# Kernel tuning notes

Hardware: AMD Instinct MI355X
Metric: run time of the kernel (lower is better)

Reference implementation:

```python
import jax, jax.numpy as jnp
import numpy as np

N_NODES = 100000
N_EDGES = 1600000
IN_FEATS = 256
HEADS = 4
OUT_FEATS = 32
NEG_SLOPE = 0.2


def setup_inputs() -> dict:
    key = jax.random.key(0)
    k = jax.random.split(key, 7)
    feat = jax.random.normal(k[0], (N_NODES, IN_FEATS), dtype=jnp.float32)
    src = jax.random.randint(k[1], (N_EDGES,), 0, N_NODES)
    dst = jax.random.randint(k[2], (N_EDGES,), 0, N_NODES)
    W = jax.random.normal(k[3], (HEADS * OUT_FEATS, IN_FEATS), dtype=jnp.float32) * 0.05
    attn_l = jax.random.normal(k[4], (1, HEADS, OUT_FEATS), dtype=jnp.float32) * 0.1
    attn_r = jax.random.normal(k[5], (1, HEADS, OUT_FEATS), dtype=jnp.float32) * 0.1
    bias = jnp.zeros((HEADS * OUT_FEATS,), dtype=jnp.float32)
    return {"feat": feat, "src": src, "dst": dst, "W": W,
            "attn_l": attn_l, "attn_r": attn_r, "bias": bias}


def reference(feat, src, dst, W, attn_l, attn_r, bias):
    N = feat.shape[0]
    H, F = attn_l.shape[1], attn_l.shape[2]
    # linear projection: [N, H*F] -> [N, H, F]
    ft = (feat @ W.T).reshape(N, H, F)
    # per-node attention scores [N, H]
    el = jnp.sum(ft * attn_l, axis=-1)
    er = jnp.sum(ft * attn_r, axis=-1)
    # edge scores: u_add_v + LeakyReLU, [E, H]
    e = el[src] + er[dst]
    e = jnp.where(e >= 0, e, NEG_SLOPE * e)
    # edge softmax segmented by destination node
    emax = jax.ops.segment_max(e, dst, num_segments=N)  # [N, H]
    emax = jnp.where(jnp.isfinite(emax), emax, 0.0)
    ex = jnp.exp(e - emax[dst])  # [E, H]
    esum = jax.ops.segment_sum(ex, dst, num_segments=N)  # [N, H]
    a = ex / jnp.maximum(esum[dst], 1e-16)  # [E, H]
    # weighted scatter-sum aggregation: u_mul_e + sum
    msg = ft[src] * a[:, :, None]  # [E, H, F]
    rst = jax.ops.segment_sum(msg, dst, num_segments=N)  # [N, H, F]
    rst = rst + bias.reshape(1, H, F)
    return rst


if __name__ == "__main__":
    out = reference(**setup_inputs())
    print(out.shape, out.dtype)
```

## Files before the change

### kernel.cpp

```cpp
#include <hip/hip_runtime.h>

#define NEG_SLOPE 0.2f
#define G_SHIFT 8
#define G_SIZE  256
#define NB1     256

typedef __attribute__((ext_vector_type(8))) short short8;
typedef __attribute__((ext_vector_type(4))) float floatx4;

__device__ inline unsigned short f32_to_bf16(float f) {
    union { float f; unsigned int u; } c; c.f = f;
    unsigned int u = c.u;
    u += 0x7FFFu + ((u >> 16) & 1u);
    return (unsigned short)(u >> 16);
}
__device__ inline float bf16_lo(unsigned int u) {
    union { unsigned int u; float f; } c; c.u = u << 16; return c.f;
}
__device__ inline float bf16_hi(unsigned int u) {
    union { unsigned int u; float f; } c; c.u = u & 0xFFFF0000u; return c.f;
}

__global__ __launch_bounds__(256) void k_wconv(const float* __restrict__ W,
                                               unsigned short* __restrict__ Wb,
                                               int n) {
    int i = blockIdx.x * 256 + threadIdx.x;
    if (i < n) Wb[i] = f32_to_bf16(W[i]);
}

__global__ __launch_bounds__(256) void k_gemm_mfma(const float* __restrict__ feat,
                                                   const unsigned short* __restrict__ Wb,
                                                   unsigned short* __restrict__ ftb,
                                                   int M) {
    const int tid  = threadIdx.x;
    const int wave = tid >> 6;
    const int lane = tid & 63;
    const int l16  = lane & 15;
    const int quad = lane >> 4;
    const int mw   = blockIdx.x * 64 + wave * 16;

    int arow = mw + l16;
    if (arow >= M) arow = M - 1;
    const float* aptr = feat + (size_t)arow * 256 + quad * 8;

    floatx4 acc[8];
#pragma unroll
    for (int t = 0; t < 8; ++t) acc[t] = (floatx4){0.f, 0.f, 0.f, 0.f};

#pragma unroll
    for (int k0 = 0; k0 < 256; k0 += 32) {
        float4 a0 = *(const float4*)(aptr + k0);
        float4 a1 = *(const float4*)(aptr + k0 + 4);
        short8 af;
        af[0] = (short)f32_to_bf16(a0.x);
        af[1] = (short)f32_to_bf16(a0.y);
        af[2] = (short)f32_to_bf16(a0.z);
        af[3] = (short)f32_to_bf16(a0.w);
        af[4] = (short)f32_to_bf16(a1.x);
        af[5] = (short)f32_to_bf16(a1.y);
        af[6] = (short)f32_to_bf16(a1.z);
        af[7] = (short)f32_to_bf16(a1.w);
#pragma unroll
        for (int t = 0; t < 8; ++t) {
            short8 bf = *(const short8*)(Wb + (size_t)(t * 16 + l16) * 256 + k0 + quad * 8);
            acc[t] = __builtin_amdgcn_mfma_f32_16x16x32_bf16(af, bf, acc[t], 0, 0, 0);
        }
    }

#pragma unroll
    for (int t = 0; t < 8; ++t) {
#pragma unroll
        for (int r = 0; r < 4; ++r) {
            int row = mw + quad * 4 + r;
            if (row < M)
                ftb[(size_t)row * 128 + t * 16 + l16] = f32_to_bf16(acc[t][r]);
        }
    }
}

__global__ __launch_bounds__(256) void k_elr(const unsigned short* __restrict__ ftb,
                                             const float* __restrict__ al,
                                             const float* __restrict__ ar,
                                             float* __restrict__ el,
                                             float* __restrict__ er,
                                             int NH) {
    int i = blockIdx.x * 256 + threadIdx.x;
    if (i >= NH) return;
    int h = i & 3;
    const unsigned int* f = (const unsigned int*)ftb + (size_t)i * 16;
    const float* lp = al + h * 32;
    const float* rp = ar + h * 32;
    float sl = 0.f, sr = 0.f;
#pragma unroll
    for (int j = 0; j < 16; ++j) {
        unsigned int u = f[j];
        float f0 = bf16_lo(u), f1 = bf16_hi(u);
        sl += f0 * lp[2 * j] + f1 * lp[2 * j + 1];
        sr += f0 * rp[2 * j] + f1 * rp[2 * j + 1];
    }
    el[i] = sl;
    er[i] = sr;
}

__global__ __launch_bounds__(256) void k_count(const int* __restrict__ dst,
                                               int* __restrict__ counts,
                                               int E, int CH, int B) {
    __shared__ int hist[512];
    int j = blockIdx.x, t = threadIdx.x;
    for (int bk = t; bk < B; bk += 256) hist[bk] = 0;
    __syncthreads();
    int lo = j * CH, hi = min(E, lo + CH);
    for (int i = lo + t; i < hi; i += 256)
        atomicAdd(&hist[dst[i] >> G_SHIFT], 1);
    __syncthreads();
    for (int bk = t; bk < B; bk += 256) counts[bk * NB1 + j] = hist[bk];
}

__global__ __launch_bounds__(256) void k_scan1(const int* __restrict__ deg,
                                               int* __restrict__ offs,
                                               int* __restrict__ bsum, int n) {
    __shared__ int ls[256];
    int b = blockIdx.x, t = threadIdx.x;
    int base = b * 1024 + t * 4;
    int d0 = (base + 0 < n) ? deg[base + 0] : 0;
    int d1 = (base + 1 < n) ? deg[base + 1] : 0;
    int d2 = (base + 2 < n) ? deg[base + 2] : 0;
    int d3 = (base + 3 < n) ? deg[base + 3] : 0;
    int s = d0 + d1 + d2 + d3;
    ls[t] = s;
    __syncthreads();
    for (int o = 1; o < 256; o <<= 1) {
        int v = (t >= o) ? ls[t - o] : 0;
        __syncthreads();
        ls[t] += v;
        __syncthreads();
    }
    int excl = ls[t] - s;
    if (base + 0 < n) offs[base + 0] = excl;
    if (base + 1 < n) offs[base + 1] = excl + d0;
    if (base + 2 < n) offs[base + 2] = excl + d0 + d1;
    if (base + 3 < n) offs[base + 3] = excl + d0 + d1 + d2;
    if (t == 255) bsum[b] = ls[255];
}

__global__ __launch_bounds__(256) void k_scan2(int* __restrict__ bsum, int NB) {
    __shared__ int ls[256];
    int t = threadIdx.x;
    int v = (t < NB) ? bsum[t] : 0;
    ls[t] = v;
    __syncthreads();
    for (int o = 1; o < 256; o <<= 1) {
        int u = (t >= o) ? ls[t - o] : 0;
        __syncthreads();
        ls[t] += u;
        __syncthreads();
    }
    if (t < NB) bsum[t] = ls[t] - v;
}

__global__ __launch_bounds__(256) void k_partition(const int* __restrict__ src,
                                                   const int* __restrict__ dst,
                                                   const int* __restrict__ scanned,
                                                   const int* __restrict__ bsum,
                                                   int* __restrict__ part,
                                                   int E, int CH, int B) {
    __shared__ int curs[512];
    int j = blockIdx.x, t = threadIdx.x;
    for (int bk = t; bk < B; bk += 256) {
        int idx = bk * NB1 + j;
        curs[bk] = scanned[idx] + bsum[idx >> 10];
    }
    __syncthreads();
    int lo = j * CH, hi = min(E, lo + CH);
    for (int i = lo + t; i < hi; i += 256) {
        int d = dst[i];
        int bk = d >> G_SHIFT;
        int pos = atomicAdd(&curs[bk], 1);
        if (pos >= 0 && pos < E)
            part[pos] = ((d & (G_SIZE - 1)) << 17) | src[i];
    }
}

__global__ __launch_bounds__(256) void k_bucket(const int* __restrict__ scanned,
                                                const int* __restrict__ bsum,
                                                const int* __restrict__ part,
                                                int* __restrict__ offs,
                                                int* __restrict__ esrc,
                                                int E, int B, int N) {
    __shared__ int hist[256], ls[256], curs[256];
    int b = blockIdx.x, t = threadIdx.x;
    int i0 = b * NB1;
    int start = scanned[i0] + bsum[i0 >> 10];
    int end = E;
    if (b < B - 1) {
        int i1 = (b + 1) * NB1;
        end = scanned[i1] + bsum[i1 >> 10];
    }

    hist[t] = 0;
    __syncthreads();
    for (int i = start + t; i < end; i += 256)
        atomicAdd(&hist[(part[i] >> 17) & 255], 1);
    __syncthreads();

    int h = hist[t];
    ls[t] = h;
    __syncthreads();
    for (int o = 1; o < 256; o <<= 1) {
        int v = (t >= o) ? ls[t - o] : 0;
        __syncthreads();
        ls[t] += v;
        __syncthreads();
    }
    int excl = ls[t] - h;
    curs[t] = excl;
    int node = b * G_SIZE + t;
    if (node < N) offs[node] = start + excl;
    if (b == B - 1 && t == 0) offs[N] = E;
    __syncthreads();

    for (int i = start + t; i < end; i += 256) {
        int p = part[i];
        int pos = start + atomicAdd(&curs[(p >> 17) & 255], 1);
        if (pos >= 0 && pos < E) esrc[pos] = p & 0x1FFFF;
    }
}

__global__ __launch_bounds__(256) void k_aggr_csr(const int* __restrict__ offs,
                                                  const int* __restrict__ esrc,
                                                  const float* __restrict__ el,
                                                  const float* __restrict__ er,
                                                  const unsigned short* __restrict__ ftb,
                                                  const float* __restrict__ bias,
                                                  float* __restrict__ out,
                                                  int N) {
    int node = blockIdx.x * 4 + (threadIdx.x >> 6);
    if (node >= N) return;
    int lane = threadIdx.x & 63;
    int h1 = lane & 3;
    int h2b = (lane >> 4) << 2;
    float er1 = er[node * 4 + h1];

    int start = offs[node];
    int deg   = offs[node + 1] - start;

    float2 acc = make_float2(0.f, 0.f);
    float  wsum = 0.f;
    const unsigned int* ftu = (const unsigned int*)ftb;

    int p = 0;
    while (p < deg) {
        int cnt = min(16, deg - p);
        float w = 0.f;
        int   s = 0;
        int   e = lane >> 2;
        if (e < cnt) {
            s = esrc[start + p + e];
            float x = el[s * 4 + h1] + er1;
            x = x >= 0.f ? x : NEG_SLOPE * x;
            w = __expf(x);
        }
        float        wv[16];
        unsigned int uv[16];
#pragma unroll
        for (int j = 0; j < 16; ++j) {
            int ib = (j << 4) + h2b;
            wv[j] = __int_as_float(
                __builtin_amdgcn_ds_bpermute(ib, __float_as_int(w)));
            int sj = __builtin_amdgcn_ds_bpermute(ib, s);
            uv[j] = ftu[(size_t)sj * 64 + lane];
        }
#pragma unroll
        for (int j = 0; j < 16; ++j) {
            wsum  += wv[j];
            acc.x += wv[j] * bf16_lo(uv[j]);
            acc.y += wv[j] * bf16_hi(uv[j]);
        }
        p += cnt;
    }
    float scale = 1.0f / fmaxf(wsum, 1e-16f);
    float2 bv = ((const float2*)bias)[lane];
    float2 o;
    o.x = acc.x * scale + bv.x;
    o.y = acc.y * scale + bv.y;
    ((float2*)out)[(size_t)node * 64 + lane] = o;
}

__global__ __launch_bounds__(256) void k_init_fb(float* __restrict__ out,
                                                 const float* __restrict__ bias,
                                                 float* __restrict__ esum,
                                                 int n_out, int n_esum) {
    int i = blockIdx.x * 256 + threadIdx.x;
    if (i < n_out)  out[i]  = bias[i & 127];
    if (i < n_esum) esum[i] = 0.0f;
}

__global__ __launch_bounds__(256) void k_esum_fb(const int* __restrict__ src,
                                                 const int* __restrict__ dst,
                                                 const float* __restrict__ el,
                                                 const float* __restrict__ er,
                                                 float* __restrict__ esum,
                                                 int E4) {
    int i = blockIdx.x * 256 + threadIdx.x;
    if (i >= E4) return;
    int e = i >> 2, h = i & 3;
    int s = src[e], d = dst[e];
    float x = el[s * 4 + h] + er[d * 4 + h];
    x = x >= 0.f ? x : NEG_SLOPE * x;
    atomicAdd(&esum[d * 4 + h], __expf(x));
}

__global__ __launch_bounds__(256) void k_aggr_fb(const int* __restrict__ src,
                                                 const int* __restrict__ dst,
                                                 const float* __restrict__ el,
                                                 const float* __restrict__ er,
                                                 const float* __restrict__ esum,
                                                 const unsigned short* __restrict__ ftb,
                                                 float* __restrict__ out,
                                                 int E) {
    int i = blockIdx.x * 256 + threadIdx.x;
    int e = i >> 6;
    if (e >= E) return;
    int c = i & 63;
    int h = c >> 4;
    int s = src[e], d = dst[e];
    float x = el[s * 4 + h] + er[d * 4 + h];
    x = x >= 0.f ? x : NEG_SLOPE * x;
    float a = __expf(x) / fmaxf(esum[d * 4 + h], 1e-16f);
    unsigned int u = ((const unsigned int*)ftb)[(size_t)s * 64 + c];
    float* o = out + (size_t)d * 128 + c * 2;
    atomicAdd(o + 0, bf16_lo(u) * a);
    atomicAdd(o + 1, bf16_hi(u) * a);
}

extern "C" void kernel_launch(void* const* d_in, const int* in_sizes, int n_in,
                              void* d_out, int out_size, void* d_ws, size_t ws_size,
                              hipStream_t stream) {
    const float* feat   = (const float*)d_in[0];
    const int*   src    = (const int*)d_in[1];
    const int*   dst    = (const int*)d_in[2];
    const float* W      = (const float*)d_in[3];
    const float* attn_l = (const float*)d_in[4];
    const float* attn_r = (const float*)d_in[5];
    const float* bias   = (const float*)d_in[6];

    const int N  = in_sizes[0] / 256;
    const int E  = in_sizes[1];
    const int NW = in_sizes[3];
    float* out = (float*)d_out;

    const int B  = (N + G_SIZE - 1) / G_SIZE;
    const int CH = (E + NB1 - 1) / NB1;
    const int n2 = B * NB1;

    unsigned short* ftb = (unsigned short*)d_ws;
    unsigned short* Wb  = ftb + (size_t)N * 128;
    float* el = (float*)(Wb + NW);
    float* er = el + (size_t)N * 4;
    int* offs    = (int*)(er + (size_t)N * 4);
    int* counts  = offs + (N + 1);
    int* scanned = counts + n2;
    int* bsum    = scanned + n2;
    int* part    = bsum + 256;
    int* esrc    = part + E;
    size_t need = (size_t)((char*)(esrc + E) - (char*)d_ws);

    k_wconv<<<(NW + 255) / 256, 256, 0, stream>>>(W, Wb, NW);
    k_gemm_mfma<<<(N + 63) / 64, 256, 0, stream>>>(feat, Wb, ftb, N);
    k_elr<<<(N * 4 + 255) / 256, 256, 0, stream>>>(ftb, attn_l, attn_r, el, er, N * 4);

    if (ws_size >= need) {
        const int NBs = (n2 + 1023) / 1024;
        k_count<<<NB1, 256, 0, stream>>>(dst, counts, E, CH, B);
        k_scan1<<<NBs, 256, 0, stream>>>(counts, scanned, bsum, n2);
        k_scan2<<<1, 256, 0, stream>>>(bsum, NBs);
        k_partition<<<NB1, 256, 0, stream>>>(src, dst, scanned, bsum, part, E, CH, B);
        k_bucket<<<B, 256, 0, stream>>>(scanned, bsum, part, offs, esrc, E, B, N);
        k_aggr_csr<<<(N + 3) / 4, 256, 0, stream>>>(offs, esrc, el, er, ftb, bias, out, N);
    } else {
        float* esum = (float*)(er + (size_t)N * 4);
        k_init_fb<<<(N * 128 + 255) / 256, 256, 0, stream>>>(out, bias, esum, N * 128, N * 4);
        k_esum_fb<<<(E * 4 + 255) / 256, 256, 0, stream>>>(src, dst, el, er, esum, E * 4);
        k_aggr_fb<<<((size_t)E * 64 + 255) / 256, 256, 0, stream>>>(src, dst, el, er, esum, ftb, out, E);
    }
}
```

Before: 362.1 us.

## Stage GEMM A tiles via async global-to-LDS loads with register-resident W

The projection GEMM now keeps each wave's half of W in registers for the whole K loop. Feature rows are streamed into a 4-deep swizzled LDS ring using global_load_lds, with a three-stage prefetch and waitcnt/barrier sync. Work is also split 2x2 across waves (M by N) so the A tile is shared through LDS. The aim is to overlap feature-load latency with MFMA work and cut redundant W loads, at the cost of more registers, 32KB of LDS per block and barrier overhead, in a GEMM that is only one stage of the pipeline.

```diff
diff --git a/kernel.cpp b/kernel.cpp
--- a/kernel.cpp
+++ b/kernel.cpp
@@ -32,48 +32,100 @@
                                                    const unsigned short* __restrict__ Wb,
                                                    unsigned short* __restrict__ ftb,
                                                    int M) {
+    __shared__ float Abuf[4][2048];
+
     const int tid  = threadIdx.x;
-    const int wave = tid >> 6;
+    const int w    = tid >> 6;
     const int lane = tid & 63;
     const int l16  = lane & 15;
     const int quad = lane >> 4;
-    const int mw   = blockIdx.x * 64 + wave * 16;
-
-    int arow = mw + l16;
-    if (arow >= M) arow = M - 1;
-    const float* aptr = feat + (size_t)arow * 256 + quad * 8;
-
-    floatx4 acc[8];
-#pragma unroll
-    for (int t = 0; t < 8; ++t) acc[t] = (floatx4){0.f, 0.f, 0.f, 0.f};
-
-#pragma unroll
-    for (int k0 = 0; k0 < 256; k0 += 32) {
-        float4 a0 = *(const float4*)(aptr + k0);
-        float4 a1 = *(const float4*)(aptr + k0 + 4);
-        short8 af;
-        af[0] = (short)f32_to_bf16(a0.x);
-        af[1] = (short)f32_to_bf16(a0.y);
-        af[2] = (short)f32_to_bf16(a0.z);
-        af[3] = (short)f32_to_bf16(a0.w);
-        af[4] = (short)f32_to_bf16(a1.x);
-        af[5] = (short)f32_to_bf16(a1.y);
-        af[6] = (short)f32_to_bf16(a1.z);
-        af[7] = (short)f32_to_bf16(a1.w);
-#pragma unroll
-        for (int t = 0; t < 8; ++t) {
-            short8 bf = *(const short8*)(Wb + (size_t)(t * 16 + l16) * 256 + k0 + quad * 8);
-            acc[t] = __builtin_amdgcn_mfma_f32_16x16x32_bf16(af, bf, acc[t], 0, 0, 0);
-        }
-    }
-
-#pragma unroll
-    for (int t = 0; t < 8; ++t) {
-#pragma unroll
-        for (int r = 0; r < 4; ++r) {
-            int row = mw + quad * 4 + r;
-            if (row < M)
-                ftb[(size_t)row * 128 + t * 16 + l16] = f32_to_bf16(acc[t][r]);
+    const int wm   = w & 1;
+    const int wn   = w >> 1;
+    const int tile = blockIdx.x * 64;
+
+    short8 b[4][8];
+#pragma unroll
+    for (int t = 0; t < 4; ++t) {
+        const unsigned short* bp =
+            Wb + (size_t)((wn * 4 + t) * 16 + l16) * 256 + quad * 8;
+#pragma unroll
+        for (int kc = 0; kc < 8; ++kc)
+            b[t][kc] = *(const short8*)(bp + kc * 32);
+    }
+
+    const int rloc = lane >> 3;
+    const int c4   = ((lane & 7) ^ rloc) * 4;
+    int gr0 = tile + (w * 2 + 0) * 8 + rloc; if (gr0 >= M) gr0 = M - 1;
+    int gr1 = tile + (w * 2 + 1) * 8 + rloc; if (gr1 >= M) gr1 = M - 1;
+    const float* g0 = feat + (size_t)gr0 * 256 + c4;
+    const float* g1 = feat + (size_t)gr1 * 256 + c4;
+
+#define STAGE(JC) do {                                                          \
+    __builtin_amdgcn_global_load_lds(                                           \
+        (const __attribute__((address_space(1))) unsigned int*)(g0 + (JC) * 32),\
+        (__attribute__((address_space(3))) unsigned int*)&Abuf[(JC) & 3][(w * 2 + 0) * 256], \
+        16, 0, 0);                                                              \
+    __builtin_amdgcn_global_load_lds(                                           \
+        (const __attribute__((address_space(1))) unsigned int*)(g1 + (JC) * 32),\
+        (__attribute__((address_space(3))) unsigned int*)&Abuf[(JC) & 3][(w * 2 + 1) * 256], \
+        16, 0, 0);                                                              \
+} while (0)
+
+    floatx4 acc[2][4];
+#pragma unroll
+    for (int m = 0; m < 2; ++m)
+#pragma unroll
+        for (int t = 0; t < 4; ++t)
+            acc[m][t] = (floatx4){0.f, 0.f, 0.f, 0.f};
+
+    STAGE(0); STAGE(1); STAGE(2);
+
+    const int sw = (l16 & 7) << 4;
+
+#define KSTEP(J, VM) do {                                                       \
+    asm volatile("s_waitcnt vmcnt(" #VM ")" ::: "memory");                      \
+    __builtin_amdgcn_s_barrier();                                               \
+    asm volatile("" ::: "memory");                                              \
+    if ((J) + 3 < 8) STAGE((J) + 3);                                            \
+    const char* ab = (const char*)&Abuf[(J) & 3][0];                            \
+    _Pragma("unroll")                                                           \
+    for (int m = 0; m < 2; ++m) {                                               \
+        int base = (wm * 32 + m * 16 + l16) * 128 + quad * 32;                  \
+        float4 alo = *(const float4*)(ab + ((base)      ^ sw));                 \
+        float4 ahi = *(const float4*)(ab + ((base + 16) ^ sw));                 \
+        short8 af;                                                              \
+        af[0] = (short)f32_to_bf16(alo.x);                                      \
+        af[1] = (short)f32_to_bf16(alo.y);                                      \
+        af[2] = (short)f32_to_bf16(alo.z);                                      \
+        af[3] = (short)f32_to_bf16(alo.w);                                      \
+        af[4] = (short)f32_to_bf16(ahi.x);                                      \
+        af[5] = (short)f32_to_bf16(ahi.y);                                      \
+        af[6] = (short)f32_to_bf16(ahi.z);                                      \
+        af[7] = (short)f32_to_bf16(ahi.w);                                      \
+        _Pragma("unroll")                                                       \
+        for (int t = 0; t < 4; ++t)                                             \
+            acc[m][t] = __builtin_amdgcn_mfma_f32_16x16x32_bf16(                \
+                af, b[t][(J)], acc[m][t], 0, 0, 0);                             \
+    }                                                                           \
+} while (0)
+
+    KSTEP(0, 4); KSTEP(1, 4); KSTEP(2, 4); KSTEP(3, 4);
+    KSTEP(4, 4); KSTEP(5, 4); KSTEP(6, 2); KSTEP(7, 0);
+
+#undef KSTEP
+#undef STAGE
+
+#pragma unroll
+    for (int m = 0; m < 2; ++m) {
+#pragma unroll
+        for (int t = 0; t < 4; ++t) {
+#pragma unroll
+            for (int r = 0; r < 4; ++r) {
+                int row = tile + wm * 32 + m * 16 + quad * 4 + r;
+                if (row < M)
+                    ftb[(size_t)row * 128 + (wn * 4 + t) * 16 + l16] =
+                        f32_to_bf16(acc[m][t][r]);
+            }
         }
     }
 }
```

Measured after the change: 343.2 us. -5.2%, faster.
